# Kernel tuning notes

Measured on AMD Instinct MI355X. Metric: run time of the kernel, lower is better.

The kernel has to match this reference:

```python
import jax, jax.numpy as jnp
import numpy as np


def setup_inputs() -> dict:
    key = jax.random.key(0)
    k1, k2 = jax.random.split(key)
    Nd, Ld, E = 128, 128, 128   # docs, doc sentences, embed_size
    Nq, Lq = 128, 32            # queries, query sentences
    # ColBERT-style: embeddings are L2-normalized per sentence in embed()
    doc = jax.random.normal(k1, (Nd, Ld, E), dtype=jnp.float32)
    doc = doc / jnp.linalg.norm(doc, axis=-1, keepdims=True)
    # query embeddings are stored transposed: [Nq, E, Lq]
    q = jax.random.normal(k2, (Nq, Lq, E), dtype=jnp.float32)
    q = q / jnp.linalg.norm(q, axis=-1, keepdims=True)
    query = jnp.transpose(q, (0, 2, 1))  # [Nq, E, Lq]
    return {"doc_tokens": doc, "query_tokens": query}


def reference(doc_tokens, query_tokens):
    # max_sim(doc, query, sentence_wise=False, full_mat=True)
    # doc_tokens: [Nd, Ld, E]; query_tokens: [Nq, E, Lq]
    # scores[q,d,t,l] = sum_e doc[d,t,e] * query[q,e,l]   (bmm over cross product)
    scores = jnp.einsum('dte,qel->qdtl', doc_tokens, query_tokens)
    # max over doc tokens t, sum over query tokens l -> [Nq, Nd]
    return jnp.sum(jnp.max(scores, axis=2), axis=-1)
```

## Files before the change

kernel.cpp:

```cpp
#include <hip/hip_runtime.h>
#include <hip/hip_bf16.h>

typedef short short8 __attribute__((ext_vector_type(8)));
typedef float f32x16 __attribute__((ext_vector_type(16)));

#define ND 128
#define LD 128
#define EE 128
#define NQ 128
#define LQ 32
#define LDS_STRIDE 136
#define GDOCS 2

__global__ __launch_bounds__(256)
void qconvert_kernel(const float* __restrict__ qry, __hip_bfloat16* __restrict__ qB) {
  __shared__ float s[LQ][EE + 1];
  const int q   = blockIdx.x;
  const int tid = threadIdx.x;
  const float* src = qry + q * (EE * LQ);
  #pragma unroll
  for (int i = 0; i < 4; ++i) {
    int c = i * 256 + tid;
    int e = c >> 3;
    int l = (c & 7) << 2;
    float4 v = reinterpret_cast<const float4*>(src)[c];
    s[l + 0][e] = v.x;
    s[l + 1][e] = v.y;
    s[l + 2][e] = v.z;
    s[l + 3][e] = v.w;
  }
  __syncthreads();
  __hip_bfloat16* dst = qB + q * (LQ * EE);
  #pragma unroll
  for (int i = 0; i < 4; ++i) {
    int c = i * 256 + tid;
    int l = c >> 5;
    int e = (c & 31) << 2;
    union { ushort4 u; __hip_bfloat16 b[4]; } o;
    o.b[0] = __float2bfloat16(s[l][e + 0]);
    o.b[1] = __float2bfloat16(s[l][e + 1]);
    o.b[2] = __float2bfloat16(s[l][e + 2]);
    o.b[3] = __float2bfloat16(s[l][e + 3]);
    reinterpret_cast<ushort4*>(dst)[c] = o.u;
  }
}

__global__ __launch_bounds__(256)
void maxsim_kernel(const float* __restrict__ doc,
                   const __hip_bfloat16* __restrict__ qB,
                   float* __restrict__ out) {
  __shared__ __hip_bfloat16 sdoc[LD * LDS_STRIDE];
  const int d0   = blockIdx.x * GDOCS;
  const int qblk = blockIdx.y;
  const int tid  = threadIdx.x;
  const int wave = tid >> 6;
  const int lane = tid & 63;
  const int ln31 = lane & 31;
  const int half = lane >> 5;
  const int q0   = qblk * 8 + wave * 2;

  short8 bfrag[2][8];
  #pragma unroll
  for (int qq = 0; qq < 2; ++qq) {
    const __hip_bfloat16* qp = qB + (q0 + qq) * (LQ * EE) + ln31 * EE + half * 8;
    #pragma unroll
    for (int ks = 0; ks < 8; ++ks)
      bfrag[qq][ks] = *reinterpret_cast<const short8*>(qp + ks * 16);
  }

  #pragma unroll 1
  for (int g = 0; g < GDOCS; ++g) {
    const int d = d0 + g;
    __syncthreads();
    {
      const float4* src = reinterpret_cast<const float4*>(doc + d * (LD * EE));
      #pragma unroll 4
      for (int it = 0; it < 8; ++it) {
        int c = it * 256 + tid;
        float4 v0 = src[2 * c + 0];
        float4 v1 = src[2 * c + 1];
        union { uint4 u; __hip_bfloat16 b[8]; } o;
        o.b[0] = __float2bfloat16(v0.x);
        o.b[1] = __float2bfloat16(v0.y);
        o.b[2] = __float2bfloat16(v0.z);
        o.b[3] = __float2bfloat16(v0.w);
        o.b[4] = __float2bfloat16(v1.x);
        o.b[5] = __float2bfloat16(v1.y);
        o.b[6] = __float2bfloat16(v1.z);
        o.b[7] = __float2bfloat16(v1.w);
        *reinterpret_cast<uint4*>(&sdoc[(c >> 4) * LDS_STRIDE + ((c & 15) << 3)]) = o.u;
      }
    }
    __syncthreads();

    float colmax[2] = {-3.0e38f, -3.0e38f};

    #pragma unroll
    for (int mt = 0; mt < 4; ++mt) {
      f32x16 acc0 = {0.f, 0.f, 0.f, 0.f, 0.f, 0.f, 0.f, 0.f,
                     0.f, 0.f, 0.f, 0.f, 0.f, 0.f, 0.f, 0.f};
      f32x16 acc1 = acc0;

      #pragma unroll
      for (int ks = 0; ks < 8; ++ks) {
        short8 a = *reinterpret_cast<const short8*>(
            &sdoc[(mt * 32 + ln31) * LDS_STRIDE + ks * 16 + half * 8]);
        acc0 = __builtin_amdgcn_mfma_f32_32x32x16_bf16(a, bfrag[0][ks], acc0, 0, 0, 0);
        acc1 = __builtin_amdgcn_mfma_f32_32x32x16_bf16(a, bfrag[1][ks], acc1, 0, 0, 0);
      }

      float t0a = fmaxf(fmaxf(acc0[0], acc0[1]),  fmaxf(acc0[2], acc0[3]));
      float t0b = fmaxf(fmaxf(acc0[4], acc0[5]),  fmaxf(acc0[6], acc0[7]));
      float t0c = fmaxf(fmaxf(acc0[8], acc0[9]),  fmaxf(acc0[10], acc0[11]));
      float t0d = fmaxf(fmaxf(acc0[12], acc0[13]), fmaxf(acc0[14], acc0[15]));
      colmax[0] = fmaxf(colmax[0], fmaxf(fmaxf(t0a, t0b), fmaxf(t0c, t0d)));
      float t1a = fmaxf(fmaxf(acc1[0], acc1[1]),  fmaxf(acc1[2], acc1[3]));
      float t1b = fmaxf(fmaxf(acc1[4], acc1[5]),  fmaxf(acc1[6], acc1[7]));
      float t1c = fmaxf(fmaxf(acc1[8], acc1[9]),  fmaxf(acc1[10], acc1[11]));
      float t1d = fmaxf(fmaxf(acc1[12], acc1[13]), fmaxf(acc1[14], acc1[15]));
      colmax[1] = fmaxf(colmax[1], fmaxf(fmaxf(t1a, t1b), fmaxf(t1c, t1d)));
    }

    #pragma unroll
    for (int qq = 0; qq < 2; ++qq) {
      float m = colmax[qq];
      m = fmaxf(m, __shfl_xor(m, 32, 64));
      float s = m;
      s += __shfl_xor(s, 1, 64);
      s += __shfl_xor(s, 2, 64);
      s += __shfl_xor(s, 4, 64);
      s += __shfl_xor(s, 8, 64);
      s += __shfl_xor(s, 16, 64);
      if (lane == 0) out[(q0 + qq) * ND + d] = s;
    }
  }
}

extern "C" void kernel_launch(void* const* d_in, const int* in_sizes, int n_in,
                              void* d_out, int out_size, void* d_ws, size_t ws_size,
                              hipStream_t stream) {
  const float* doc = (const float*)d_in[0];
  const float* qry = (const float*)d_in[1];
  float* out = (float*)d_out;

  __hip_bfloat16* qB = (__hip_bfloat16*)d_ws;

  qconvert_kernel<<<dim3(NQ), dim3(256), 0, stream>>>(qry, qB);
  maxsim_kernel<<<dim3(ND / GDOCS, NQ / 8), dim3(256), 0, stream>>>(doc, qB, out);
}
```

Baseline: 81.38 us.

## Double-buffer doc halves in LDS and overlap global loads with MFMA

Splits each document into 64-row halves held in two LDS buffers. The loads for the next half are issued into registers while MFMAs run on the current half, then converted and stored to LDS. This is meant to hide global load latency behind compute instead of serializing load and compute per document. It also sets launch bounds to 4 blocks per CU, which limits registers and may cause spills, and it adds a barrier per half-segment.

```diff
diff --git a/kernel.cpp b/kernel.cpp
--- a/kernel.cpp
+++ b/kernel.cpp
@@ -9,8 +9,9 @@
 #define EE 128
 #define NQ 128
 #define LQ 32
-#define LDS_STRIDE 136
-#define GDOCS 2
+#define STRIDE 136
+#define HROWS 64
+#define HELEMS (HROWS * EE)
 
 __global__ __launch_bounds__(256)
 void qconvert_kernel(const float* __restrict__ qry, __hip_bfloat16* __restrict__ qB) {
@@ -45,94 +46,118 @@
   }
 }
 
-__global__ __launch_bounds__(256)
+__global__ __launch_bounds__(256, 4)
 void maxsim_kernel(const float* __restrict__ doc,
                    const __hip_bfloat16* __restrict__ qB,
                    float* __restrict__ out) {
-  __shared__ __hip_bfloat16 sdoc[LD * LDS_STRIDE];
-  const int d0   = blockIdx.x * GDOCS;
+  __shared__ __hip_bfloat16 sdoc[2][HROWS * STRIDE];
+  const int d0   = blockIdx.x * 2;
   const int qblk = blockIdx.y;
   const int tid  = threadIdx.x;
   const int wave = tid >> 6;
   const int lane = tid & 63;
   const int ln31 = lane & 31;
-  const int half = lane >> 5;
+  const int kh   = lane >> 5;
   const int q0   = qblk * 8 + wave * 2;
 
   short8 bfrag[2][8];
   #pragma unroll
   for (int qq = 0; qq < 2; ++qq) {
-    const __hip_bfloat16* qp = qB + (q0 + qq) * (LQ * EE) + ln31 * EE + half * 8;
+    const __hip_bfloat16* qp = qB + (q0 + qq) * (LQ * EE) + ln31 * EE + kh * 8;
     #pragma unroll
     for (int ks = 0; ks < 8; ++ks)
       bfrag[qq][ks] = *reinterpret_cast<const short8*>(qp + ks * 16);
   }
 
-  #pragma unroll 1
-  for (int g = 0; g < GDOCS; ++g) {
-    const int d = d0 + g;
-    __syncthreads();
-    {
-      const float4* src = reinterpret_cast<const float4*>(doc + d * (LD * EE));
-      #pragma unroll 4
-      for (int it = 0; it < 8; ++it) {
-        int c = it * 256 + tid;
-        float4 v0 = src[2 * c + 0];
-        float4 v1 = src[2 * c + 1];
-        union { uint4 u; __hip_bfloat16 b[8]; } o;
-        o.b[0] = __float2bfloat16(v0.x);
-        o.b[1] = __float2bfloat16(v0.y);
-        o.b[2] = __float2bfloat16(v0.z);
-        o.b[3] = __float2bfloat16(v0.w);
-        o.b[4] = __float2bfloat16(v1.x);
-        o.b[5] = __float2bfloat16(v1.y);
-        o.b[6] = __float2bfloat16(v1.z);
-        o.b[7] = __float2bfloat16(v1.w);
-        *reinterpret_cast<uint4*>(&sdoc[(c >> 4) * LDS_STRIDE + ((c & 15) << 3)]) = o.u;
-      }
+  float4 pf[4];
+  float colmax0 = -3.0e38f, colmax1 = -3.0e38f;
+
+  auto issue = [&](int seg, int grp) {
+    const float4* src = reinterpret_cast<const float4*>(
+        doc + (d0 + (seg >> 1)) * (LD * EE) + (seg & 1) * HELEMS);
+    #pragma unroll
+    for (int i = 0; i < 2; ++i) {
+      int c = (grp * 2 + i) * 256 + tid;
+      pf[2 * i]     = src[2 * c];
+      pf[2 * i + 1] = src[2 * c + 1];
     }
-    __syncthreads();
+  };
+  auto flush = [&](int seg, int grp) {
+    __hip_bfloat16* dst = sdoc[seg & 1];
+    #pragma unroll
+    for (int i = 0; i < 2; ++i) {
+      int c = (grp * 2 + i) * 256 + tid;
+      float4 v0 = pf[2 * i], v1 = pf[2 * i + 1];
+      union { uint4 u; __hip_bfloat16 b[8]; } o;
+      o.b[0] = __float2bfloat16(v0.x);
+      o.b[1] = __float2bfloat16(v0.y);
+      o.b[2] = __float2bfloat16(v0.z);
+      o.b[3] = __float2bfloat16(v0.w);
+      o.b[4] = __float2bfloat16(v1.x);
+      o.b[5] = __float2bfloat16(v1.y);
+      o.b[6] = __float2bfloat16(v1.z);
+      o.b[7] = __float2bfloat16(v1.w);
+      *reinterpret_cast<uint4*>(&dst[(c >> 4) * STRIDE + ((c & 15) << 3)]) = o.u;
+    }
+  };
+  auto compute_mt = [&](int seg, int mt) {
+    const __hip_bfloat16* sp = sdoc[seg & 1];
+    f32x16 acc0 = {0.f, 0.f, 0.f, 0.f, 0.f, 0.f, 0.f, 0.f,
+                   0.f, 0.f, 0.f, 0.f, 0.f, 0.f, 0.f, 0.f};
+    f32x16 acc1 = acc0;
+    #pragma unroll
+    for (int ks = 0; ks < 8; ++ks) {
+      short8 a = *reinterpret_cast<const short8*>(
+          &sp[(mt * 32 + ln31) * STRIDE + ks * 16 + kh * 8]);
+      acc0 = __builtin_amdgcn_mfma_f32_32x32x16_bf16(a, bfrag[0][ks], acc0, 0, 0, 0);
+      acc1 = __builtin_amdgcn_mfma_f32_32x32x16_bf16(a, bfrag[1][ks], acc1, 0, 0, 0);
+    }
+    float t0 = fmaxf(fmaxf(fmaxf(acc0[0], acc0[1]), fmaxf(acc0[2], acc0[3])),
+                     fmaxf(fmaxf(acc0[4], acc0[5]), fmaxf(acc0[6], acc0[7])));
+    float u0 = fmaxf(fmaxf(fmaxf(acc0[8], acc0[9]), fmaxf(acc0[10], acc0[11])),
+                     fmaxf(fmaxf(acc0[12], acc0[13]), fmaxf(acc0[14], acc0[15])));
+    colmax0 = fmaxf(colmax0, fmaxf(t0, u0));
+    float t1 = fmaxf(fmaxf(fmaxf(acc1[0], acc1[1]), fmaxf(acc1[2], acc1[3])),
+                     fmaxf(fmaxf(acc1[4], acc1[5]), fmaxf(acc1[6], acc1[7])));
+    float u1 = fmaxf(fmaxf(fmaxf(acc1[8], acc1[9]), fmaxf(acc1[10], acc1[11])),
+                     fmaxf(fmaxf(acc1[12], acc1[13]), fmaxf(acc1[14], acc1[15])));
+    colmax1 = fmaxf(colmax1, fmaxf(t1, u1));
+  };
 
-    float colmax[2] = {-3.0e38f, -3.0e38f};
+  issue(0, 0); flush(0, 0);
+  issue(0, 1); flush(0, 1);
+  __syncthreads();
 
-    #pragma unroll
-    for (int mt = 0; mt < 4; ++mt) {
-      f32x16 acc0 = {0.f, 0.f, 0.f, 0.f, 0.f, 0.f, 0.f, 0.f,
-                     0.f, 0.f, 0.f, 0.f, 0.f, 0.f, 0.f, 0.f};
-      f32x16 acc1 = acc0;
+  #pragma unroll
+  for (int seg = 0; seg < 4; ++seg) {
+    if (seg < 3) issue(seg + 1, 0);
+    compute_mt(seg, 0);
+    if (seg < 3) { flush(seg + 1, 0); issue(seg + 1, 1); }
+    compute_mt(seg, 1);
+    if (seg < 3) flush(seg + 1, 1);
 
-      #pragma unroll
-      for (int ks = 0; ks < 8; ++ks) {
-        short8 a = *reinterpret_cast<const short8*>(
-            &sdoc[(mt * 32 + ln31) * LDS_STRIDE + ks * 16 + half * 8]);
-        acc0 = __builtin_amdgcn_mfma_f32_32x32x16_bf16(a, bfrag[0][ks], acc0, 0, 0, 0);
-        acc1 = __builtin_amdgcn_mfma_f32_32x32x16_bf16(a, bfrag[1][ks], acc1, 0, 0, 0);
-      }
-
-      float t0a = fmaxf(fmaxf(acc0[0], acc0[1]),  fmaxf(acc0[2], acc0[3]));
-      float t0b = fmaxf(fmaxf(acc0[4], acc0[5]),  fmaxf(acc0[6], acc0[7]));
-      float t0c = fmaxf(fmaxf(acc0[8], acc0[9]),  fmaxf(acc0[10], acc0[11]));
-      float t0d = fmaxf(fmaxf(acc0[12], acc0[13]), fmaxf(acc0[14], acc0[15]));
-      colmax[0] = fmaxf(colmax[0], fmaxf(fmaxf(t0a, t0b), fmaxf(t0c, t0d)));
-      float t1a = fmaxf(fmaxf(acc1[0], acc1[1]),  fmaxf(acc1[2], acc1[3]));
-      float t1b = fmaxf(fmaxf(acc1[4], acc1[5]),  fmaxf(acc1[6], acc1[7]));
-      float t1c = fmaxf(fmaxf(acc1[8], acc1[9]),  fmaxf(acc1[10], acc1[11]));
-      float t1d = fmaxf(fmaxf(acc1[12], acc1[13]), fmaxf(acc1[14], acc1[15]));
-      colmax[1] = fmaxf(colmax[1], fmaxf(fmaxf(t1a, t1b), fmaxf(t1c, t1d)));
-    }
-
-    #pragma unroll
-    for (int qq = 0; qq < 2; ++qq) {
-      float m = colmax[qq];
-      m = fmaxf(m, __shfl_xor(m, 32, 64));
+    if (seg & 1) {
+      const int d = d0 + (seg >> 1);
+      float m = fmaxf(colmax0, __shfl_xor(colmax0, 32, 64));
       float s = m;
       s += __shfl_xor(s, 1, 64);
       s += __shfl_xor(s, 2, 64);
       s += __shfl_xor(s, 4, 64);
       s += __shfl_xor(s, 8, 64);
       s += __shfl_xor(s, 16, 64);
-      if (lane == 0) out[(q0 + qq) * ND + d] = s;
+      if (lane == 0) out[q0 * ND + d] = s;
+      float m1 = fmaxf(colmax1, __shfl_xor(colmax1, 32, 64));
+      float s1 = m1;
+      s1 += __shfl_xor(s1, 1, 64);
+      s1 += __shfl_xor(s1, 2, 64);
+      s1 += __shfl_xor(s1, 4, 64);
+      s1 += __shfl_xor(s1, 8, 64);
+      s1 += __shfl_xor(s1, 16, 64);
+      if (lane == 0) out[(q0 + 1) * ND + d] = s1;
+      colmax0 = -3.0e38f;
+      colmax1 = -3.0e38f;
     }
+    __syncthreads();
   }
 }
 
@@ -146,5 +171,5 @@
   __hip_bfloat16* qB = (__hip_bfloat16*)d_ws;
 
   qconvert_kernel<<<dim3(NQ), dim3(256), 0, stream>>>(qry, qB);
-  maxsim_kernel<<<dim3(ND / GDOCS, NQ / 8), dim3(256), 0, stream>>>(doc, qB, out);
+  maxsim_kernel<<<dim3(ND / 2, NQ / 8), dim3(256), 0, stream>>>(doc, qB, out);
 }
```

New measurement: 119.2 us. 1.46x slower.
